# Optimization experiments

Hardware: AMD Instinct MI355X
Metric: run time of the kernel (lower is better)

The kernel has to match this reference:

```python
import jax, jax.numpy as jnp
import numpy as np

COST_CLASS, COST_BBOX, COST_GIOU = 2.0, 5.0, 2.0
ALPHA, GAMMA = 0.25, 2.0
EPS = 1e-8
N_CANDIDATE = 10


def box_cxcywh_to_xyxy(b):
    cx, cy, w, h = b[..., 0], b[..., 1], b[..., 2], b[..., 3]
    return jnp.stack([cx - 0.5 * w, cy - 0.5 * h, cx + 0.5 * w, cy + 0.5 * h], axis=-1)


def pairwise_iou_giou(b1, b2):
    # b1: [N,4] xyxy, b2: [M,4] xyxy -> iou [N,M], giou [N,M]
    area1 = (b1[:, 2] - b1[:, 0]) * (b1[:, 3] - b1[:, 1])
    area2 = (b2[:, 2] - b2[:, 0]) * (b2[:, 3] - b2[:, 1])
    lt = jnp.maximum(b1[:, None, :2], b2[None, :, :2])
    rb = jnp.minimum(b1[:, None, 2:], b2[None, :, 2:])
    wh = jnp.clip(rb - lt, 0.0)
    inter = wh[..., 0] * wh[..., 1]
    union = area1[:, None] + area2[None, :] - inter
    iou = inter / (union + EPS)
    # smallest enclosing box
    lt_c = jnp.minimum(b1[:, None, :2], b2[None, :, :2])
    rb_c = jnp.maximum(b1[:, None, 2:], b2[None, :, 2:])
    wh_c = jnp.clip(rb_c - lt_c, 0.0)
    area_c = wh_c[..., 0] * wh_c[..., 1]
    giou = iou - (area_c - union) / (area_c + EPS)
    return iou, giou


def _match_one(logits, boxes, labels, tboxes):
    # logits [Q,C], boxes [Q,4] cxcywh, labels [G] int, tboxes [G,4] cxcywh
    Q = logits.shape[0]
    G = labels.shape[0]
    prob = jax.nn.sigmoid(logits)                 # [Q,C]  (use_focal_loss path)
    p = prob[:, labels]                           # [Q,G] gather at GT classes
    neg_cost = (1.0 - ALPHA) * p ** GAMMA * (-jnp.log1p(-p + EPS))
    pos_cost = ALPHA * (1.0 - p) ** GAMMA * (-jnp.log(p + EPS))
    cost_class = pos_cost - neg_cost              # [Q,G]
    cost_bbox = jnp.sum(jnp.abs(boxes[:, None, :] - tboxes[None, :, :]), axis=-1)  # L1 cdist [Q,G]
    iou, giou = pairwise_iou_giou(box_cxcywh_to_xyxy(boxes), box_cxcywh_to_xyxy(tboxes))
    C = COST_BBOX * cost_bbox + COST_CLASS * cost_class + COST_GIOU * (-giou)      # [Q,G]

    # --- SimOTA matching (simota_matching), vectorized over GT ---
    cost = C.T                                    # [G,Q]
    ious = iou.T                                  # [G,Q]
    n_cand = min(N_CANDIDATE, Q)
    topk_ious, _ = jax.lax.top_k(ious, n_cand)    # [G,n_cand]
    dynamic_ks = jnp.clip(jnp.sum(topk_ious, axis=1).astype(jnp.int32), 1)  # [G]
    # rank of each anchor per GT under ascending cost
    ranks = jnp.argsort(jnp.argsort(cost, axis=1), axis=1)                  # [G,Q]
    matching = (ranks < dynamic_ks[:, None]).astype(cost.dtype)             # [G,Q]
    # resolve anchors matched to multiple GTs: keep argmin-cost GT
    anchor_matching_gt = matching.sum(axis=0)     # [Q]
    cost_argmin = jnp.argmin(cost, axis=0)        # [Q]
    onehot_min = (jnp.arange(G)[:, None] == cost_argmin[None, :]).astype(cost.dtype)
    matching = jnp.where(anchor_matching_gt[None, :] > 1, onehot_min, matching)
    return jnp.stack([cost, matching], axis=0)    # [2,G,Q]


def reference(pred_logits, pred_boxes, tgt_labels, tgt_boxes):
    # per-image cost blocks + SimOTA matching matrices: [bs, 2, G, Q]
    return jax.vmap(_match_one)(pred_logits, pred_boxes, tgt_labels, tgt_boxes)


def setup_inputs() -> dict:
    key = jax.random.key(0)
    k1, k2, k3, k4 = jax.random.split(key, 4)
    bs, Q, C, G = 16, 4000, 80, 128
    pred_logits = jax.random.normal(k1, (bs, Q, C), dtype=jnp.float32)
    pred_boxes = jax.random.uniform(k2, (bs, Q, 4), dtype=jnp.float32, minval=0.05, maxval=0.95)
    tgt_labels = jax.random.randint(k3, (bs, G), 0, C)
    tgt_boxes = jax.random.uniform(k4, (bs, G, 4), dtype=jnp.float32, minval=0.05, maxval=0.95)
    return {"pred_logits": pred_logits, "pred_boxes": pred_boxes,
            "tgt_labels": tgt_labels, "tgt_boxes": tgt_boxes}
```

## Files before the change

kernel.cpp:

```cpp
#include <hip/hip_runtime.h>
#include <cmath>
#include <cfloat>
#include <climits>


static constexpr int BS = 16;
static constexpr int Qn = 4000;
static constexpr int Cn = 80;
static constexpr int Gn = 128;
static constexpr float kEPS = 1e-8f;


static constexpr size_t kThrvOff = 0;
static constexpr size_t kThriOff = 8 * 1024;
static constexpr size_t kFOff    = 16 * 1024;
static constexpr size_t kFBytes  = (size_t)BS * Cn * Qn * sizeof(float);

__device__ __forceinline__ float focal_cost(float l) {
    const float p = 1.0f / (1.0f + expf(-l));
    const float neg = (0.75f * (p * p)) * (-log1pf(-p + kEPS));
    const float pos = (0.25f * ((1.0f - p) * (1.0f - p))) * (-logf(p + kEPS));
    return pos - neg;
}

__global__ __launch_bounds__(256) void kP_focal(
    const float* __restrict__ logits,
    float* __restrict__ F)
{
    const int b  = blockIdx.y;
    const int q0 = blockIdx.x * 32;
    const int t  = threadIdx.x;

    __shared__ float s_f[32 * 81];

    const float* src = logits + ((size_t)b * Qn + q0) * Cn;
#pragma unroll
    for (int i = 0; i < 10; ++i) {
        const int idx = t + i * 256;
        const int ql = idx / 80, c = idx % 80;
        s_f[ql * 81 + c] = focal_cost(src[idx]);
    }
    __syncthreads();

    float* dst = F + (size_t)b * Cn * Qn;
#pragma unroll
    for (int i = 0; i < 10; ++i) {
        const int j = t + i * 256;
        const int c = j >> 5, ql = j & 31;
        dst[(size_t)c * Qn + q0 + ql] = s_f[ql * 81 + c];
    }
}

__device__ __forceinline__ unsigned long long pack_ci(float c, int q) {
    const unsigned int u = __float_as_uint(c + 0.0f);
    const unsigned int s = (u & 0x80000000u) ? ~u : (u | 0x80000000u);
    return ((unsigned long long)s << 32) | (unsigned int)q;
}

__device__ __forceinline__ unsigned long long shfl_xor_u64(unsigned long long v, int m) {
    const int lo = __shfl_xor((int)(unsigned int)v, m, 64);
    const int hi = __shfl_xor((int)(unsigned int)(v >> 32), m, 64);
    return ((unsigned long long)(unsigned int)hi << 32) | (unsigned int)lo;
}

__device__ __forceinline__ unsigned long long bitonic64_asc_u64(unsigned long long v, int lane) {
#pragma unroll
    for (int k = 2; k <= 64; k <<= 1) {
#pragma unroll
        for (int j = 32; j >= 1; j >>= 1) {
            if (j < k) {
                const unsigned long long o = shfl_xor_u64(v, j);
                const bool up = ((lane & k) == 0);
                const bool keepmin = (((lane & j) == 0) == up);
                const bool omin = (o < v);
                v = (keepmin == omin) ? o : v;
            }
        }
    }
    return v;
}

__device__ __forceinline__ float bitonic64_asc_f32(float v, int lane) {
#pragma unroll
    for (int k = 2; k <= 64; k <<= 1) {
#pragma unroll
        for (int j = 32; j >= 1; j >>= 1) {
            if (j < k) {
                const float o = __shfl_xor(v, j, 64);
                const bool up = ((lane & k) == 0);
                const bool keepmin = (((lane & j) == 0) == up);
                const bool omin = (o < v);
                v = (keepmin == omin) ? o : v;
            }
        }
    }
    return v;
}

__device__ __forceinline__ void ins10_vi(float (&cv)[10], int (&ci)[10],
                                         float v, int q) {
    bool le[10];
#pragma unroll
    for (int j = 0; j < 10; ++j) le[j] = (cv[j] <= v);
#pragma unroll
    for (int j = 9; j >= 1; --j) {
        const float nv = le[j] ? cv[j] : (le[j - 1] ? v : cv[j - 1]);
        const int   ni = le[j] ? ci[j] : (le[j - 1] ? q : ci[j - 1]);
        cv[j] = nv; ci[j] = ni;
    }
    if (!le[0]) { cv[0] = v; ci[0] = q; }
}

__device__ __forceinline__ void ins10_desc(float (&iv)[10], float v) {
    bool ge[10];
#pragma unroll
    for (int j = 0; j < 10; ++j) ge[j] = (iv[j] >= v);
#pragma unroll
    for (int j = 9; j >= 1; --j)
        iv[j] = ge[j] ? iv[j] : (ge[j - 1] ? v : iv[j - 1]);
    if (!ge[0]) iv[0] = v;
}

template <bool USE_F>
__global__ __launch_bounds__(512, 8) void kF(
    const float* __restrict__ boxes,
    const int*   __restrict__ labels,
    const float* __restrict__ tboxes,
    const float* __restrict__ logits,
    const float* __restrict__ F,
    float* __restrict__ out,
    float* __restrict__ thrv,
    int*   __restrict__ thri)
{
    const int lane = threadIdx.x & 63;
    const int w8   = threadIdx.x >> 6;
    const int sub  = w8 & 3;
    const int r    = blockIdx.x;
    const int b    = r >> 7;
    const int g    = r & (Gn - 1);

    const float* tb = tboxes + (size_t)r * 4;
    const float tcx = tb[0], tcy = tb[1], tw = tb[2], th = tb[3];
    const float tx0 = tcx - 0.5f * tw, ty0 = tcy - 0.5f * th;
    const float tx1 = tcx + 0.5f * tw, ty1 = tcy + 0.5f * th;
    const float tarea = (tx1 - tx0) * (ty1 - ty0);

    const float4* brow = reinterpret_cast<const float4*>(boxes) + (size_t)b * Qn;
    const int lab = labels[r];
    const float* Frow = USE_F ? (F + ((size_t)b * Cn + lab) * Qn) : nullptr;
    const float* lcol = USE_F ? nullptr : (logits + (size_t)b * Qn * Cn + lab);
    float* crow = out + (size_t)(b * 2) * Gn * Qn + (size_t)g * Qn;

    __shared__ float              s_cost[4096];
    __shared__ float              s_iou[4096];
    __shared__ unsigned long long s_ccb[4][64];
    __shared__ float              s_icb[4][64];
    __shared__ int                s_cnt[8];
    __shared__ unsigned long long s_ce[4][12];
    __shared__ float              s_if[4][12];
    __shared__ float              s_T[8];

    if (lane == 0) s_cnt[w8] = 0;

    float trk = (w8 < 4) ? INFINITY : -INFINITY;

#pragma unroll
    for (int it = 0; it < 2; ++it) {
        const int q0 = w8 * 512 + it * 256 + (lane << 2);
        if ((it == 0) || (q0 < Qn)) {
            float cls4[4];
            if (USE_F) {
                const float4 f4 = *reinterpret_cast<const float4*>(Frow + q0);
                cls4[0] = f4.x; cls4[1] = f4.y; cls4[2] = f4.z; cls4[3] = f4.w;
            } else {
#pragma unroll
                for (int e = 0; e < 4; ++e)
                    cls4[e] = focal_cost(lcol[(size_t)(q0 + e) * Cn]);
            }
            float c4[4], io4[4];
#pragma unroll
            for (int e = 0; e < 4; ++e) {
                const float cls = cls4[e];
                const float4 bb = brow[q0 + e];
                const float cx = bb.x, cy = bb.y, w = bb.z, h = bb.w;
                const float x0 = cx - 0.5f * w, y0 = cy - 0.5f * h;
                const float x1 = cx + 0.5f * w, y1 = cy + 0.5f * h;
                const float area1 = (x1 - x0) * (y1 - y0);
                const float l1 = ((fabsf(cx - tcx) + fabsf(cy - tcy))
                                  + fabsf(w - tw)) + fabsf(h - th);
                const float ltx = fmaxf(x0, tx0), lty = fmaxf(y0, ty0);
                const float rbx = fminf(x1, tx1), rby = fminf(y1, ty1);
                const float iw = fmaxf(rbx - ltx, 0.0f), ih = fmaxf(rby - lty, 0.0f);
                const float inter = iw * ih;
                const float uni = (area1 + tarea) - inter;
                const float iou = inter / (uni + kEPS);
                const float cltx = fminf(x0, tx0), clty = fminf(y0, ty0);
                const float crbx = fmaxf(x1, tx1), crby = fmaxf(y1, ty1);
                const float cw = fmaxf(crbx - cltx, 0.0f), ch = fmaxf(crby - clty, 0.0f);
                const float areac = cw * ch;
                const float giou = iou - (areac - uni) / (areac + kEPS);

                const float cost = (5.0f * l1 + 2.0f * cls) + 2.0f * (-giou);
                c4[e] = cost; io4[e] = iou;
            }
            if (w8 < 4) {
                trk = fminf(trk, fminf(fminf(c4[0], c4[1]), fminf(c4[2], c4[3])));
            } else {
                trk = fmaxf(trk, fmaxf(fmaxf(io4[0], io4[1]), fmaxf(io4[2], io4[3])));
            }
            float4 cv4; cv4.x = c4[0]; cv4.y = c4[1]; cv4.z = c4[2]; cv4.w = c4[3];
            float4 iv4; iv4.x = io4[0]; iv4.y = io4[1]; iv4.z = io4[2]; iv4.w = io4[3];
            *reinterpret_cast<float4*>(crow + q0) = cv4;
            *reinterpret_cast<float4*>(&s_cost[q0]) = cv4;
            *reinterpret_cast<float4*>(&s_iou[q0]) = iv4;
        } else {
            float4 pi; pi.x = INFINITY; pi.y = INFINITY; pi.z = INFINITY; pi.w = INFINITY;
            float4 ni; ni.x = -INFINITY; ni.y = -INFINITY; ni.z = -INFINITY; ni.w = -INFINITY;
            *reinterpret_cast<float4*>(&s_cost[q0]) = pi;
            *reinterpret_cast<float4*>(&s_iou[q0]) = ni;
        }
    }

    const float sorted = bitonic64_asc_f32(trk, lane);
    const float Tw = __shfl(sorted, (w8 < 4) ? 9 : 54, 64);
    if (lane == 0) s_T[w8] = Tw;
    __syncthreads();

    if (w8 < 4) {
        const float T = fminf(fminf(s_T[0], s_T[1]), fminf(s_T[2], s_T[3]));
        const int base = sub * 1024;
#pragma unroll
        for (int it = 0; it < 4; ++it) {
            const int idx = base + it * 256 + (lane << 2);
            const float4 c4 = *reinterpret_cast<const float4*>(&s_cost[idx]);
#pragma unroll
            for (int e = 0; e < 4; ++e) {
                const float c = (e == 0) ? c4.x : (e == 1) ? c4.y
                              : (e == 2) ? c4.z : c4.w;
                if (c <= T) {
                    const int slot = atomicAdd(&s_cnt[w8], 1);
                    if (slot < 64) s_ccb[sub][slot] = pack_ci(c, idx + e);
                }
            }
        }

        const int cnt = s_cnt[w8];
        if (cnt <= 64) {
            unsigned long long v = (lane < cnt) ? s_ccb[sub][lane] : ~0ull;
            v = bitonic64_asc_u64(v, lane);
            if (lane < 12) s_ce[sub][lane] = (lane < 10) ? v : ~0ull;
        } else {
            float cv[10]; int ci[10];
#pragma unroll
            for (int j = 0; j < 10; ++j) { cv[j] = INFINITY; ci[j] = INT_MAX; }
#pragma unroll
            for (int it = 0; it < 4; ++it) {
                const int idx = base + it * 256 + (lane << 2);
                const float4 c4 = *reinterpret_cast<const float4*>(&s_cost[idx]);
                ins10_vi(cv, ci, c4.x, idx);
                ins10_vi(cv, ci, c4.y, idx + 1);
                ins10_vi(cv, ci, c4.z, idx + 2);
                ins10_vi(cv, ci, c4.w, idx + 3);
            }
#pragma unroll
            for (int t = 0; t < 10; ++t) {
                float m = cv[0];
#pragma unroll
                for (int d = 1; d <= 32; d <<= 1)
                    m = fminf(m, __shfl_xor(m, d, 64));
                int cq = (cv[0] == m) ? ci[0] : INT_MAX;
#pragma unroll
                for (int d = 1; d <= 32; d <<= 1)
                    cq = min(cq, __shfl_xor(cq, d, 64));
                if (lane == 0) s_ce[sub][t] = pack_ci(m, cq);
                const bool own = (cv[0] == m) && (ci[0] == cq);
                if (own) {
#pragma unroll
                    for (int j = 0; j < 9; ++j) { cv[j] = cv[j + 1]; ci[j] = ci[j + 1]; }
                    cv[9] = INFINITY; ci[9] = INT_MAX;
                }
            }
            if (lane < 2) s_ce[sub][10 + lane] = ~0ull;
        }
    } else {
        const float T = fmaxf(fmaxf(s_T[4], s_T[5]), fmaxf(s_T[6], s_T[7]));
        const int base = sub * 1024;
#pragma unroll
        for (int it = 0; it < 4; ++it) {
            const int idx = base + it * 256 + (lane << 2);
            const float4 i4 = *reinterpret_cast<const float4*>(&s_iou[idx]);
#pragma unroll
            for (int e = 0; e < 4; ++e) {
                const float v = (e == 0) ? i4.x : (e == 1) ? i4.y
                              : (e == 2) ? i4.z : i4.w;
                if (v >= T) {
                    const int slot = atomicAdd(&s_cnt[w8], 1);
                    if (slot < 64) s_icb[sub][slot] = v;
                }
            }
        }

        const int cnt = s_cnt[w8];
        if (cnt <= 64) {
            float v = (lane < cnt) ? s_icb[sub][lane] : -INFINITY;
            v = bitonic64_asc_f32(v, lane);
            if (lane >= 54) s_if[sub][63 - lane] = v;
            if (lane < 2) s_if[sub][10 + lane] = -INFINITY;
        } else {
            float iv[10];
#pragma unroll
            for (int j = 0; j < 10; ++j) iv[j] = -INFINITY;
#pragma unroll
            for (int it = 0; it < 4; ++it) {
                const int idx = base + it * 256 + (lane << 2);
                const float4 i4 = *reinterpret_cast<const float4*>(&s_iou[idx]);
                ins10_desc(iv, i4.x);
                ins10_desc(iv, i4.y);
                ins10_desc(iv, i4.z);
                ins10_desc(iv, i4.w);
            }
#pragma unroll
            for (int t = 0; t < 10; ++t) {
                float m = iv[0];
#pragma unroll
                for (int d = 1; d <= 32; d <<= 1)
                    m = fmaxf(m, __shfl_xor(m, d, 64));
                if (lane == 0) s_if[sub][t] = m;
                const bool own0 = (iv[0] == m);
                const unsigned long long bal = __ballot(own0);
                if (own0 && lane == __ffsll((long long)bal) - 1) {
#pragma unroll
                    for (int j = 0; j < 9; ++j) iv[j] = iv[j + 1];
                    iv[9] = -INFINITY;
                }
            }
            if (lane < 2) s_if[sub][10 + lane] = -INFINITY;
        }
    }

    __syncthreads();

    if (threadIdx.x == 0) {
        int p0 = 0, p1 = 0, p2 = 0, p3 = 0;
        float s = 0.0f;
#pragma unroll
        for (int t = 0; t < 10; ++t) {
            const float a0 = s_if[0][p0], a1 = s_if[1][p1];
            const float a2 = s_if[2][p2], a3 = s_if[3][p3];
            const float mx = fmaxf(fmaxf(a0, a1), fmaxf(a2, a3));
            if (a0 == mx) ++p0;
            else if (a1 == mx) ++p1;
            else if (a2 == mx) ++p2;
            else ++p3;
            s += mx;
        }
        int k = (int)s;
        if (k < 1) k = 1;
        if (k > 10) k = 10;

        p0 = 0; p1 = 0; p2 = 0; p3 = 0;
        unsigned long long key = 0;
#pragma unroll
        for (int t = 0; t < 10; ++t) {
            const unsigned long long a0 = s_ce[0][p0], a1 = s_ce[1][p1];
            const unsigned long long a2 = s_ce[2][p2], a3 = s_ce[3][p3];
            unsigned long long mn = a0;
            if (a1 < mn) mn = a1;
            if (a2 < mn) mn = a2;
            if (a3 < mn) mn = a3;
            if (a0 == mn) ++p0;
            else if (a1 == mn) ++p1;
            else if (a2 == mn) ++p2;
            else ++p3;
            if (t == k - 1) key = mn;
        }
        const unsigned int su = (unsigned int)(key >> 32);
        thrv[r] = __uint_as_float((su & 0x80000000u) ? (su ^ 0x80000000u) : ~su);
        thri[r] = (int)(unsigned int)key;
    }
}

__global__ __launch_bounds__(512) void kC5(
    const float* __restrict__ outc,
    const float* __restrict__ thrv,
    const int*   __restrict__ thri,
    float* __restrict__ out)
{
    const int b    = blockIdx.y;
    const int lane = threadIdx.x & 63;
    const int gh   = threadIdx.x >> 6;
    const int quad = blockIdx.x * 64 + lane;
    const int q0   = quad * 4;

    __shared__ float              s_tv[Gn];
    __shared__ int                s_ti[Gn];
    __shared__ unsigned long long s_mask[8][64];
    __shared__ float              s_mv0[8][64], s_mv1[8][64];
    __shared__ float              s_mv2[8][64], s_mv3[8][64];
    __shared__ unsigned           s_mg[8][64];

    if (threadIdx.x < Gn) {
        s_tv[threadIdx.x] = thrv[b * Gn + threadIdx.x];
        s_ti[threadIdx.x] = thri[b * Gn + threadIdx.x];
    }
    __syncthreads();

    const bool act = (quad < Qn / 4);
    const int gbase = gh * 16;
    unsigned long long mask = 0;
    float mv0 = INFINITY, mv1 = INFINITY, mv2 = INFINITY, mv3 = INFINITY;
    int mg0 = 0, mg1 = 0, mg2 = 0, mg3 = 0;

    if (act) {
        const float* crow = outc + (size_t)(b * 2) * Gn * Qn + q0;
#pragma unroll
        for (int j = 0; j < 16; ++j) {
            const int g = gbase + j;
            const float4 c = *reinterpret_cast<const float4*>(crow + (size_t)g * Qn);
            const float tvg = s_tv[g];
            const int   tig = s_ti[g];
            const bool t0 = (c.x < tvg) || (c.x == tvg && q0     <= tig);
            const bool t1 = (c.y < tvg) || (c.y == tvg && q0 + 1 <= tig);
            const bool t2 = (c.z < tvg) || (c.z == tvg && q0 + 2 <= tig);
            const bool t3 = (c.w < tvg) || (c.w == tvg && q0 + 3 <= tig);
            mask |= ((unsigned long long)t0 << j)
                  | ((unsigned long long)t1 << (16 + j))
                  | ((unsigned long long)t2 << (32 + j))
                  | ((unsigned long long)t3 << (48 + j));
            if (c.x < mv0) { mv0 = c.x; mg0 = g; }
            if (c.y < mv1) { mv1 = c.y; mg1 = g; }
            if (c.z < mv2) { mv2 = c.z; mg2 = g; }
            if (c.w < mv3) { mv3 = c.w; mg3 = g; }
        }
    }
    s_mask[gh][lane] = mask;
    s_mv0[gh][lane] = mv0; s_mv1[gh][lane] = mv1;
    s_mv2[gh][lane] = mv2; s_mv3[gh][lane] = mv3;
    s_mg[gh][lane] = (unsigned)mg0 | ((unsigned)mg1 << 8)
                   | ((unsigned)mg2 << 16) | ((unsigned)mg3 << 24);
    __syncthreads();

    int c0 = 0, c1 = 0, c2 = 0, c3 = 0;
#pragma unroll
    for (int h = 0; h < 8; ++h) {
        const unsigned long long m = s_mask[h][lane];
        c0 += __popcll(m & 0xFFFFull);
        c1 += __popcll((m >> 16) & 0xFFFFull);
        c2 += __popcll((m >> 32) & 0xFFFFull);
        c3 += __popcll((m >> 48) & 0xFFFFull);
    }
    float b0 = s_mv0[0][lane], b1 = s_mv1[0][lane];
    float b2 = s_mv2[0][lane], b3 = s_mv3[0][lane];
    unsigned pk = s_mg[0][lane];
    int g0b = pk & 0xFF, g1b = (pk >> 8) & 0xFF;
    int g2b = (pk >> 16) & 0xFF, g3b = (pk >> 24) & 0xFF;
#pragma unroll
    for (int h = 1; h < 8; ++h) {
        const unsigned pkh = s_mg[h][lane];
        const float v0 = s_mv0[h][lane];
        if (v0 < b0) { b0 = v0; g0b = pkh & 0xFF; }
        const float v1 = s_mv1[h][lane];
        if (v1 < b1) { b1 = v1; g1b = (pkh >> 8) & 0xFF; }
        const float v2 = s_mv2[h][lane];
        if (v2 < b2) { b2 = v2; g2b = (pkh >> 16) & 0xFF; }
        const float v3 = s_mv3[h][lane];
        if (v3 < b3) { b3 = v3; g3b = (pkh >> 24) & 0xFF; }
    }
    const bool f0 = (c0 > 1), f1 = (c1 > 1), f2 = (c2 > 1), f3 = (c3 > 1);

    if (act) {
        float* mrow = out + (size_t)(b * 2 + 1) * Gn * Qn + q0;
#pragma unroll
        for (int j = 0; j < 16; ++j) {
            const int g = gbase + j;
            float4 o;
            o.x = (f0 ? (g == g0b) : ((mask >> j) & 1ull))        ? 1.0f : 0.0f;
            o.y = (f1 ? (g == g1b) : ((mask >> (16 + j)) & 1ull)) ? 1.0f : 0.0f;
            o.z = (f2 ? (g == g2b) : ((mask >> (32 + j)) & 1ull)) ? 1.0f : 0.0f;
            o.w = (f3 ? (g == g3b) : ((mask >> (48 + j)) & 1ull)) ? 1.0f : 0.0f;
            *reinterpret_cast<float4*>(mrow + (size_t)g * Qn) = o;
        }
    }
}

extern "C" void kernel_launch(void* const* d_in, const int* in_sizes, int n_in,
                              void* d_out, int out_size, void* d_ws, size_t ws_size,
                              hipStream_t stream) {
    (void)in_sizes; (void)n_in; (void)out_size;
    const float* logits = (const float*)d_in[0];
    const float* boxes  = (const float*)d_in[1];
    const int*   labels = (const int*)d_in[2];
    const float* tboxes = (const float*)d_in[3];
    float* out = (float*)d_out;

    float* thrv = (float*)((char*)d_ws + kThrvOff);
    int*   thri = (int*)  ((char*)d_ws + kThriOff);
    float* F    = (float*)((char*)d_ws + kFOff);

    const bool use_f = (ws_size >= kFOff + kFBytes);

    dim3 gF(BS * Gn);
    if (use_f) {
        dim3 gP(Qn / 32, BS);
        kP_focal<<<gP, 256, 0, stream>>>(logits, F);
        kF<true><<<gF, 512, 0, stream>>>(boxes, labels, tboxes, logits, F,
                                         out, thrv, thri);
    } else {
        kF<false><<<gF, 512, 0, stream>>>(boxes, labels, tboxes, logits, nullptr,
                                          out, thrv, thri);
    }

    dim3 gC((Qn / 4 + 63) / 64, BS);
    kC5<<<gC, 512, 0, stream>>>(out, thrv, thri, out);
}
```

Baseline: 67.94 us.

## Record per-anchor GT claims via atomics and resolve matching sparsely

During the top-k selection in kF, each GT atomically adds a packed count and GT index into a per-anchor claim word. The claim buffer is zeroed in the focal precompute kernel. A new kernel kM2 reads one claim word per anchor, so the threshold-compare mask pass of kC5 is no longer needed: it takes the single claimant directly and scans cost columns for argmin only when the count exceeds one. This adds scattered atomics and needs extra workspace, and the packed 8-bit count relies on fewer than 256 claims per anchor.

```diff
diff --git a/kernel.cpp b/kernel.cpp
--- a/kernel.cpp
+++ b/kernel.cpp
@@ -11,10 +11,12 @@
 static constexpr float kEPS = 1e-8f;
 
 
-static constexpr size_t kThrvOff = 0;
-static constexpr size_t kThriOff = 8 * 1024;
-static constexpr size_t kFOff    = 16 * 1024;
-static constexpr size_t kFBytes  = (size_t)BS * Cn * Qn * sizeof(float);
+static constexpr size_t kThrvOff  = 0;
+static constexpr size_t kThriOff  = 8 * 1024;
+static constexpr size_t kFOff     = 16 * 1024;
+static constexpr size_t kFBytes   = (size_t)BS * Cn * Qn * sizeof(float);
+static constexpr size_t kClaimOff = kFOff + kFBytes;
+static constexpr size_t kClaimBytes = (size_t)BS * Qn * sizeof(unsigned);
 
 __device__ __forceinline__ float focal_cost(float l) {
     const float p = 1.0f / (1.0f + expf(-l));
@@ -25,11 +27,15 @@
 
 __global__ __launch_bounds__(256) void kP_focal(
     const float* __restrict__ logits,
-    float* __restrict__ F)
+    float* __restrict__ F,
+    unsigned* __restrict__ claims)
 {
     const int b  = blockIdx.y;
     const int q0 = blockIdx.x * 32;
     const int t  = threadIdx.x;
+
+    if (claims != nullptr && t < 32)
+        claims[(size_t)b * Qn + q0 + t] = 0u;
 
     __shared__ float s_f[32 * 81];
 
@@ -130,7 +136,8 @@
     const float* __restrict__ F,
     float* __restrict__ out,
     float* __restrict__ thrv,
-    int*   __restrict__ thri)
+    int*   __restrict__ thri,
+    unsigned* __restrict__ claims)
 {
     const int lane = threadIdx.x & 63;
     const int w8   = threadIdx.x >> 6;
@@ -373,10 +380,47 @@
             else if (a2 == mn) ++p2;
             else ++p3;
             if (t == k - 1) key = mn;
+            if (claims != nullptr && t < k) {
+                const int q = (int)(unsigned int)mn;
+                atomicAdd(&claims[(size_t)b * Qn + q], 1u | ((unsigned)g << 8));
+            }
         }
         const unsigned int su = (unsigned int)(key >> 32);
         thrv[r] = __uint_as_float((su & 0x80000000u) ? (su ^ 0x80000000u) : ~su);
         thri[r] = (int)(unsigned int)key;
+    }
+}
+
+__global__ __launch_bounds__(512) void kM2(
+    const float* __restrict__ outc,
+    const unsigned* __restrict__ claims,
+    float* __restrict__ out)
+{
+    const int b    = blockIdx.y;
+    const int lane = threadIdx.x & 63;
+    const int gh   = threadIdx.x >> 6;
+    const int q    = blockIdx.x * 64 + lane;
+    if (q >= Qn) return;
+
+    const unsigned v = claims[(size_t)b * Qn + q];
+    const unsigned cnt = v & 0xFFu;
+    int tg = -1;
+    if (cnt == 1u) {
+        tg = (int)(v >> 8);
+    } else if (cnt > 1u) {
+        const float* crow = outc + (size_t)(b * 2) * Gn * Qn + q;
+        float mv = INFINITY;
+        for (int gg = 0; gg < Gn; ++gg) {
+            const float c = crow[(size_t)gg * Qn];
+            if (c < mv) { mv = c; tg = gg; }
+        }
+    }
+
+    float* plane = out + (size_t)(b * 2 + 1) * Gn * Qn + q;
+    const int gbase = gh * 16;
+#pragma unroll
+    for (int j = 0; j < 16; ++j) {
+        plane[(size_t)(gbase + j) * Qn] = ((gbase + j) == tg) ? 1.0f : 0.0f;
     }
 }
 
@@ -493,23 +537,33 @@
     const float* tboxes = (const float*)d_in[3];
     float* out = (float*)d_out;
 
-    float* thrv = (float*)((char*)d_ws + kThrvOff);
-    int*   thri = (int*)  ((char*)d_ws + kThriOff);
-    float* F    = (float*)((char*)d_ws + kFOff);
-
-    const bool use_f = (ws_size >= kFOff + kFBytes);
+    float*    thrv   = (float*)   ((char*)d_ws + kThrvOff);
+    int*      thri   = (int*)     ((char*)d_ws + kThriOff);
+    float*    F      = (float*)   ((char*)d_ws + kFOff);
+    unsigned* claims = (unsigned*)((char*)d_ws + kClaimOff);
+
+    const bool use_f  = (ws_size >= kFOff + kFBytes);
+    const bool sparse = (ws_size >= kClaimOff + kClaimBytes);
 
     dim3 gF(BS * Gn);
-    if (use_f) {
+    if (use_f && sparse) {
         dim3 gP(Qn / 32, BS);
-        kP_focal<<<gP, 256, 0, stream>>>(logits, F);
+        kP_focal<<<gP, 256, 0, stream>>>(logits, F, claims);
         kF<true><<<gF, 512, 0, stream>>>(boxes, labels, tboxes, logits, F,
-                                         out, thrv, thri);
+                                         out, thrv, thri, claims);
+        dim3 gM((Qn + 63) / 64, BS);
+        kM2<<<gM, 512, 0, stream>>>(out, claims, out);
+    } else if (use_f) {
+        dim3 gP(Qn / 32, BS);
+        kP_focal<<<gP, 256, 0, stream>>>(logits, F, nullptr);
+        kF<true><<<gF, 512, 0, stream>>>(boxes, labels, tboxes, logits, F,
+                                         out, thrv, thri, nullptr);
+        dim3 gC((Qn / 4 + 63) / 64, BS);
+        kC5<<<gC, 512, 0, stream>>>(out, thrv, thri, out);
     } else {
         kF<false><<<gF, 512, 0, stream>>>(boxes, labels, tboxes, logits, nullptr,
-                                          out, thrv, thri);
-    }
-
-    dim3 gC((Qn / 4 + 63) / 64, BS);
-    kC5<<<gC, 512, 0, stream>>>(out, thrv, thri, out);
-}
+                                          out, thrv, thri, nullptr);
+        dim3 gC((Qn / 4 + 63) / 64, BS);
+        kC5<<<gC, 512, 0, stream>>>(out, thrv, thri, out);
+    }
+}
```

After: 74.21 us. +9.2%, slower.
